# Optimization experiments

Measured on AMD Instinct MI355X. Metric: run time of the kernel, lower is better.

The kernel has to match this reference:

```python
import jax, jax.numpy as jnp
import numpy as np

B, H, L, V = 128, 1024, 60, 50257


def setup_inputs() -> dict:
    key = jax.random.key(0)
    ks = jax.random.split(key, 14)
    s = 0.02
    f32 = jnp.float32
    return {
        "input": jax.random.randint(ks[0], (B,), 0, V),
        "hidden": jax.random.normal(ks[1], (1, B, H), f32),
        "encoder_outputs": jax.random.normal(ks[2], (B, L, H), f32),
        # learned parameters
        "emb": (jax.random.normal(ks[3], (V, H), f32) * s),
        "attn_W": (jax.random.normal(ks[4], (L, 2 * H), f32) * s),
        "attn_b": jnp.zeros((L,), f32),
        "comb_W": (jax.random.normal(ks[5], (H, 2 * H), f32) * s),
        "comb_b": jnp.zeros((H,), f32),
        "W_ih": (jax.random.normal(ks[6], (3 * H, H), f32) * s),
        "W_hh": (jax.random.normal(ks[7], (3 * H, H), f32) * s),
        "b_ih": jnp.zeros((3 * H,), f32),
        "b_hh": jnp.zeros((3 * H,), f32),
        "out_W": (jax.random.normal(ks[8], (V, H), f32) * s),
        "out_b": jnp.zeros((V,), f32),
    }


def reference(input, hidden, encoder_outputs, emb, attn_W, attn_b,
              comb_W, comb_b, W_ih, W_hh, b_ih, b_hh, out_W, out_b):
    # embedding lookup (dropout is identity in eval mode)
    embedded = emb[input]                      # [B, H]
    h = hidden[0]                              # [B, H]

    # Bahdanau-style attention over fixed max_length positions
    attn_logits = jnp.concatenate([embedded, h], axis=1) @ attn_W.T + attn_b  # [B, L]
    attn_weights = jax.nn.softmax(attn_logits, axis=1)                        # [B, L]
    attn_applied = jnp.einsum('bl,blh->bh', attn_weights, encoder_outputs)    # [B, H]

    # combine + relu
    x = jnp.concatenate([embedded, attn_applied], axis=1) @ comb_W.T + comb_b  # [B, H]
    x = jax.nn.relu(x)

    # single GRU step (PyTorch gate order: r, z, n)
    gi = x @ W_ih.T + b_ih                     # [B, 3H]
    gh = h @ W_hh.T + b_hh                     # [B, 3H]
    i_r, i_z, i_n = jnp.split(gi, 3, axis=1)
    h_r, h_z, h_n = jnp.split(gh, 3, axis=1)
    r = jax.nn.sigmoid(i_r + h_r)
    z = jax.nn.sigmoid(i_z + h_z)
    n = jnp.tanh(i_n + r * h_n)
    h_new = (1.0 - z) * n + z * h              # [B, H]

    # output projection + log_softmax over vocab
    logp = jax.nn.log_softmax(h_new @ out_W.T + out_b, axis=1)  # [B, V]
    return logp, h_new[None], attn_weights
```

## Files before the change

kernel.cpp:

```cpp
#include <hip/hip_runtime.h>
#include <hip/hip_bf16.h>

#define B_ 128
#define H_ 1024
#define L_ 60
#define V_ 50257

typedef __attribute__((ext_vector_type(8))) short bf16x8;
typedef __attribute__((ext_vector_type(4))) float f32x4;

__device__ __forceinline__ unsigned short f2bf(float f) {
  union { __hip_bfloat16 h; unsigned short u; } v;
  v.h = __float2bfloat16(f);
  return v.u;
}

__device__ __forceinline__ bf16x8 cvt8(float4 a, float4 b) {
  union { bf16x8 v; __hip_bfloat16 h[8]; } u;
  u.h[0] = __float2bfloat16(a.x); u.h[1] = __float2bfloat16(a.y);
  u.h[2] = __float2bfloat16(a.z); u.h[3] = __float2bfloat16(a.w);
  u.h[4] = __float2bfloat16(b.x); u.h[5] = __float2bfloat16(b.y);
  u.h[6] = __float2bfloat16(b.z); u.h[7] = __float2bfloat16(b.w);
  return u.v;
}

#define SBAR()   __builtin_amdgcn_s_barrier()
#define SCHED0() __builtin_amdgcn_sched_barrier(0)
__device__ __forceinline__ void lwait0() { asm volatile("s_waitcnt lgkmcnt(0)" ::: "memory"); }

__device__ __forceinline__ size_t packIdx(int b, int k) {
  int s = k >> 5;
  int bm = b >> 4;
  int lane = (b & 15) | (((k >> 3) & 3) << 4);
  return ((size_t)((s * 8 + bm) * 64 + lane) << 3) | (size_t)(k & 7);
}

__global__ __launch_bounds__(256) void k_front(
    const int* __restrict__ input, const float* __restrict__ hidden,
    const float* __restrict__ emb, const float* __restrict__ attn_W,
    const float* __restrict__ attn_b, unsigned short* __restrict__ aXa,
    unsigned short* __restrict__ aH, float* __restrict__ lbuf)
{
  int bx = blockIdx.x;
  if (bx < 512) {
    int idx = bx * 256 + threadIdx.x;
    int b = idx >> 10, j = idx & (H_ - 1);
    float e = emb[(size_t)input[b] * H_ + j];
    float h = hidden[idx];
    size_t p = packIdx(b, j);
    aXa[p] = f2bf(e);
    aH[p]  = f2bf(h);
  } else {
    int t = threadIdx.x, wv = t >> 6, lane = t & 63;
    int task = (bx - 512) * 4 + wv;
    int b = task / L_, l = task - b * L_;
    const float* erow = emb + (size_t)input[b] * H_;
    const float* hrow = hidden + (size_t)b * H_;
    const float* wr = attn_W + (size_t)l * (2 * H_);
    float acc = 0.f;
    #pragma unroll 4
    for (int i = 0; i < 16; ++i) {
      int m = lane + i * 64;
      acc += erow[m] * wr[m] + hrow[m] * wr[H_ + m];
    }
    #pragma unroll
    for (int off = 32; off; off >>= 1) acc += __shfl_xor(acc, off);
    if (lane == 0) lbuf[b * 64 + l] = acc + attn_b[l];
  }
}

__global__ __launch_bounds__(256) void k_appsm(
    const float* __restrict__ enc, const float* __restrict__ lbuf,
    float* __restrict__ attnw, unsigned short* __restrict__ aXa)
{
  __shared__ float sWt[64];
  int b = blockIdx.x, q = blockIdx.y, t = threadIdx.x;
  if (t < 64) {
    float v = (t < L_) ? lbuf[b * 64 + t] : -1e30f;
    float m = v;
    #pragma unroll
    for (int off = 32; off; off >>= 1) m = fmaxf(m, __shfl_xor(m, off));
    float e = (t < L_) ? __expf(v - m) : 0.f;
    float s = e;
    #pragma unroll
    for (int off = 32; off; off >>= 1) s += __shfl_xor(s, off);
    float w = e / s;
    sWt[t] = w;
    if (q == 0 && t < L_) attnw[b * L_ + t] = w;
  }
  __syncthreads();
  int col = q * 256 + t;
  const float* eb = enc + (size_t)b * L_ * H_ + col;
  float acc = 0.f;
  #pragma unroll 4
  for (int l = 0; l < L_; ++l) acc += sWt[l] * eb[(size_t)l * H_];
  aXa[packIdx(b, H_ + col)] = f2bf(acc);
}

__global__ __launch_bounds__(256, 4) void k_gemm(
    const unsigned short* __restrict__ Apk, const unsigned short* __restrict__ Apk2,
    const float* __restrict__ Wt, const float* __restrict__ Wt2,
    const float* __restrict__ bias, float* __restrict__ Cdir,
    float* __restrict__ Cpart, float* __restrict__ Cpart2,
    float* __restrict__ pms, int K, int N, int nchunks, int halfY, int nblkx)
{
  __shared__ __align__(16) unsigned short bufW0[64 * 32];
  __shared__ __align__(16) unsigned short bufW1[64 * 32];
  int t = threadIdx.x, wv = t >> 6, lane = t & 63;
  int y = blockIdx.y;
  const unsigned short* A = Apk;
  const float* W = Wt;
  float* CP = Cpart;
  int sidx = y;
  if (halfY && y >= halfY) { A = Apk2; W = Wt2; CP = Cpart2; sidx = y - halfY; }
  int chunk0 = sidx * nchunks;
  int n0 = blockIdx.x * 64;
  int ch = wv & 1;
  int bm0 = (wv >> 1) * 4;
  int g = lane >> 4;

  int sr  = wv * 16 + (lane >> 2);
  int sj  = lane & 3;
  int ssl = sj ^ ((sr >> 1) & 3);
  int sgcol = n0 + sr; sgcol = (sgcol < N) ? sgcol : (N - 1);
  const float* wsrc = W + (size_t)sgcol * K + sj * 8;
  unsigned short* wdst0 = &bufW0[sr * 32 + ssl * 8];
  unsigned short* wdst1 = &bufW1[sr * 32 + ssl * 8];

  f32x4 acc[4][2];
  #pragma unroll
  for (int i = 0; i < 4; ++i)
    #pragma unroll
    for (int j = 0; j < 2; ++j) acc[i][j] = (f32x4){0.f, 0.f, 0.f, 0.f};

  auto GW = [&](int kc, float4& lo, float4& hi) {
    const float* p = wsrc + (size_t)kc * 32;
    lo = *(const float4*)p;
    hi = *(const float4*)(p + 4);
  };
  const bf16x8* apg = (const bf16x8*)A;
  auto LA = [&](int kc, bf16x8* x) {
    #pragma unroll
    for (int j = 0; j < 4; ++j)
      x[j] = apg[((size_t)kc * 8 + bm0 + j) * 64 + lane];
  };
  auto COMP = [&](const unsigned short* buf, const bf16x8* a) {
    #pragma unroll
    for (int nci = 0; nci < 2; ++nci) {
      int rr = (ch * 2 + nci) * 16 + (lane & 15);
      int s = g ^ ((rr >> 1) & 3);
      bf16x8 bfr = *(const bf16x8*)&buf[rr * 32 + s * 8];
      #pragma unroll
      for (int j = 0; j < 4; ++j)
        acc[j][nci] = __builtin_amdgcn_mfma_f32_16x16x32_bf16(a[j], bfr, acc[j][nci], 0, 0, 0);
    }
  };

  float4 lo0, hi0, lo1, hi1;
  bf16x8 aA[4], aB[4];
  GW(chunk0, lo0, hi0); LA(chunk0, aA);

  for (int kk = 0; kk < nchunks; kk += 2) {
    if (kk + 1 < nchunks) { GW(chunk0 + kk + 1, lo1, hi1); LA(chunk0 + kk + 1, aB); }
    *(bf16x8*)wdst0 = cvt8(lo0, hi0);
    lwait0(); SCHED0(); SBAR(); SCHED0();
    COMP(bufW0, aA);
    if (kk + 1 >= nchunks) break;
    if (kk + 2 < nchunks) { GW(chunk0 + kk + 2, lo0, hi0); LA(chunk0 + kk + 2, aA); }
    *(bf16x8*)wdst1 = cvt8(lo1, hi1);
    lwait0(); SCHED0(); SBAR(); SCHED0();
    COMP(bufW1, aB);
  }

  int cols[2]; float bv[2];
  #pragma unroll
  for (int nci = 0; nci < 2; ++nci) {
    int c = n0 + (ch * 2 + nci) * 16 + (lane & 15);
    cols[nci] = c;
    bv[nci] = (bias && c < N) ? bias[c] : 0.f;
  }
  int rb = (lane >> 4) * 4;
  if (CP) {
    float* dst = CP + (size_t)sidx * B_ * N;
    #pragma unroll
    for (int bm = 0; bm < 4; ++bm)
      #pragma unroll
      for (int r = 0; r < 4; ++r) {
        int row = (bm0 + bm) * 16 + rb + r;
        #pragma unroll
        for (int nci = 0; nci < 2; ++nci)
          if (cols[nci] < N) dst[(size_t)row * N + cols[nci]] = acc[bm][nci][r];
      }
  } else {
    #pragma unroll
    for (int bm = 0; bm < 4; ++bm)
      #pragma unroll
      for (int r = 0; r < 4; ++r) {
        int row = (bm0 + bm) * 16 + rb + r;
        #pragma unroll
        for (int nci = 0; nci < 2; ++nci)
          if (cols[nci] < N) Cdir[(size_t)row * N + cols[nci]] = acc[bm][nci][r] + bv[nci];
      }
    if (pms) {
      #pragma unroll
      for (int bm = 0; bm < 4; ++bm)
        #pragma unroll
        for (int r = 0; r < 4; ++r) {
          int row = (bm0 + bm) * 16 + rb + r;
          float m = -1e30f;
          #pragma unroll
          for (int nci = 0; nci < 2; ++nci)
            if (cols[nci] < N) m = fmaxf(m, acc[bm][nci][r] + bv[nci]);
          #pragma unroll
          for (int off = 8; off; off >>= 1) m = fmaxf(m, __shfl_xor(m, off));
          float e = 0.f;
          #pragma unroll
          for (int nci = 0; nci < 2; ++nci)
            if (cols[nci] < N) e += __expf(acc[bm][nci][r] + bv[nci] - m);
          #pragma unroll
          for (int off = 8; off; off >>= 1) e += __shfl_xor(e, off);
          if ((lane & 15) == 0) {
            size_t o = ((size_t)row * (2 * nblkx) + blockIdx.x * 2 + ch) * 2;
            pms[o] = m; pms[o + 1] = e;
          }
        }
    }
  }
}

__global__ __launch_bounds__(256) void k_reduce_comb(
    const float* __restrict__ parts, const float* __restrict__ bias,
    unsigned short* __restrict__ aX)
{
  int idx = blockIdx.x * 256 + threadIdx.x;
  int b = idx >> 10, j = idx & (H_ - 1);
  float s = bias[j];
  #pragma unroll
  for (int p = 0; p < 16; ++p) s += parts[(size_t)p * B_ * H_ + idx];
  s = fmaxf(s, 0.f);
  aX[packIdx(b, j)] = f2bf(s);
}

__global__ __launch_bounds__(256) void k_gate(
    const float* __restrict__ giP, const float* __restrict__ ghP,
    const float* __restrict__ b_ih, const float* __restrict__ b_hh,
    const float* __restrict__ hidden, float* __restrict__ hnew,
    unsigned short* __restrict__ aHn)
{
  int idx = blockIdx.x * 256 + threadIdx.x;
  int b = idx >> 10, j = idx & (H_ - 1);
  size_t base = (size_t)b * 3 * H_;
  float ir = b_ih[j], iz = b_ih[H_ + j], in_ = b_ih[2 * H_ + j];
  float hr = b_hh[j], hz = b_hh[H_ + j], hn = b_hh[2 * H_ + j];
  #pragma unroll
  for (int p = 0; p < 4; ++p) {
    const float* gi = giP + (size_t)p * B_ * 3 * H_ + base;
    const float* gh = ghP + (size_t)p * B_ * 3 * H_ + base;
    ir += gi[j]; iz += gi[H_ + j]; in_ += gi[2 * H_ + j];
    hr += gh[j]; hz += gh[H_ + j]; hn += gh[2 * H_ + j];
  }
  float r = 1.f / (1.f + __expf(-(ir + hr)));
  float z = 1.f / (1.f + __expf(-(iz + hz)));
  float n = tanhf(in_ + r * hn);
  float h = hidden[idx];
  float hv = (1.f - z) * n + z * h;
  hnew[idx] = hv;
  aHn[packIdx(b, j)] = f2bf(hv);
}

#define SL_ 6283
__global__ __launch_bounds__(256) void k_lsub(
    float* __restrict__ logits, const float* __restrict__ pms, int nblk2)
{
  __shared__ float sm[4], ss[4], sc;
  int b = blockIdx.x, sl = blockIdx.y, t = threadIdx.x;
  float M = -1e30f, S = 0.f;
  for (int i = t; i < nblk2; i += 256) {
    float m = pms[((size_t)b * nblk2 + i) * 2];
    float s = pms[((size_t)b * nblk2 + i) * 2 + 1];
    float nm = fmaxf(M, m);
    S = S * __expf(M - nm) + s * __expf(m - nm);
    M = nm;
  }
  #pragma unroll
  for (int off = 32; off; off >>= 1) {
    float m2 = __shfl_xor(M, off), s2 = __shfl_xor(S, off);
    float nm = fmaxf(M, m2);
    S = S * __expf(M - nm) + s2 * __expf(m2 - nm);
    M = nm;
  }
  if ((t & 63) == 0) { sm[t >> 6] = M; ss[t >> 6] = S; }
  __syncthreads();
  if (t == 0) {
    float Mf = sm[0], Sf = ss[0];
    #pragma unroll
    for (int i = 1; i < 4; ++i) {
      float nm = fmaxf(Mf, sm[i]);
      Sf = Sf * __expf(Mf - nm) + ss[i] * __expf(sm[i] - nm);
      Mf = nm;
    }
    sc = Mf + logf(Sf);
  }
  __syncthreads();
  float c = sc;
  int v0 = sl * SL_;
  int v1 = v0 + SL_; if (v1 > V_) v1 = V_;
  float* row = logits + (size_t)b * V_;
  for (int v = v0 + t; v < v1; v += 256) row[v] -= c;
}

extern "C" void kernel_launch(void* const* d_in, const int* in_sizes, int n_in,
                              void* d_out, int out_size, void* d_ws, size_t ws_size,
                              hipStream_t stream)
{
  const int*   input  = (const int*)d_in[0];
  const float* hidden = (const float*)d_in[1];
  const float* enc    = (const float*)d_in[2];
  const float* emb    = (const float*)d_in[3];
  const float* attn_W = (const float*)d_in[4];
  const float* attn_b = (const float*)d_in[5];
  const float* comb_W = (const float*)d_in[6];
  const float* comb_b = (const float*)d_in[7];
  const float* W_ih   = (const float*)d_in[8];
  const float* W_hh   = (const float*)d_in[9];
  const float* b_ih   = (const float*)d_in[10];
  const float* b_hh   = (const float*)d_in[11];
  const float* out_W  = (const float*)d_in[12];
  const float* out_b  = (const float*)d_in[13];

  float* out    = (float*)d_out;
  float* logits = out;
  float* hnew   = out + (size_t)B_ * V_;
  float* attnw  = hnew + (size_t)B_ * H_;

  const int NBLK = (V_ + 63) / 64;
  char* ws = (char*)d_ws;
  unsigned short* aXa = (unsigned short*)(ws);
  unsigned short* aH  = (unsigned short*)(ws + 524288);
  unsigned short* aX  = (unsigned short*)(ws + 786432);
  unsigned short* aHn = (unsigned short*)(ws + 1048576);
  float* lbuf  = (float*)(ws + 1310720);
  float* pms   = (float*)(ws + 1343488);
  float* combP = (float*)(ws + 4194304);
  float* giP   = (float*)(ws + 4194304);
  float* ghP   = (float*)(ws + 4194304 + 6291456);

  k_front<<<512 + (B_ * L_) / 4, 256, 0, stream>>>(input, hidden, emb, attn_W, attn_b,
                                                   aXa, aH, lbuf);
  k_appsm<<<dim3(B_, 4), 256, 0, stream>>>(enc, lbuf, attnw, aXa);
  k_gemm<<<dim3(16, 16), 256, 0, stream>>>(aXa, nullptr, comb_W, nullptr, nullptr,
                                           nullptr, combP, nullptr, nullptr,
                                           2 * H_, H_, 4, 0, 0);
  k_reduce_comb<<<(B_ * H_) / 256, 256, 0, stream>>>(combP, comb_b, aX);
  k_gemm<<<dim3(48, 8), 256, 0, stream>>>(aX, aH, W_ih, W_hh, nullptr,
                                          nullptr, giP, ghP, nullptr,
                                          H_, 3 * H_, 8, 4, 0);
  k_gate<<<(B_ * H_) / 256, 256, 0, stream>>>(giP, ghP, b_ih, b_hh, hidden, hnew, aHn);
  k_gemm<<<dim3(NBLK, 1), 256, 0, stream>>>(aHn, nullptr, out_W, nullptr, out_b,
                                            logits, nullptr, nullptr, pms,
                                            H_, V_, 32, 0, NBLK);
  k_lsub<<<dim3(B_, 8), 256, 0, stream>>>(logits, pms, 2 * NBLK);
}
```

Before: 131.9 us.

## Stage activations via global_load_lds and narrow GEMM tiles to 32 columns

The shared GEMM kernel now loads the packed bf16 activation tiles directly into LDS with global_load_lds instead of into registers. It runs a deeper 4-stage register prefetch of the fp32 weights, with vmcnt-based waits. The N tile shrinks from 64 to 32 columns, which doubles the block count for all three GEMMs, and launch bounds rise to 6 blocks per SM. The aim is better latency hiding and occupancy on the bandwidth-bound out_W projection, at the cost of more redundant activation traffic per block and more barriers. The pms buffer moves because it grows to hold twice as many partial entries.

```diff
diff --git a/kernel.cpp b/kernel.cpp
--- a/kernel.cpp
+++ b/kernel.cpp
@@ -7,6 +7,7 @@
 #define V_ 50257
 
 typedef __attribute__((ext_vector_type(8))) short bf16x8;
+typedef __attribute__((ext_vector_type(4))) short bf16x4;
 typedef __attribute__((ext_vector_type(4))) float f32x4;
 
 __device__ __forceinline__ unsigned short f2bf(float f) {
@@ -15,18 +16,17 @@
   return v.u;
 }
 
-__device__ __forceinline__ bf16x8 cvt8(float4 a, float4 b) {
-  union { bf16x8 v; __hip_bfloat16 h[8]; } u;
-  u.h[0] = __float2bfloat16(a.x); u.h[1] = __float2bfloat16(a.y);
-  u.h[2] = __float2bfloat16(a.z); u.h[3] = __float2bfloat16(a.w);
-  u.h[4] = __float2bfloat16(b.x); u.h[5] = __float2bfloat16(b.y);
-  u.h[6] = __float2bfloat16(b.z); u.h[7] = __float2bfloat16(b.w);
-  return u.v;
+__device__ __forceinline__ void gl_lds16(const void* g, void* l) {
+  __builtin_amdgcn_global_load_lds(
+      (const __attribute__((address_space(1))) unsigned int*)g,
+      (__attribute__((address_space(3))) unsigned int*)l, 16, 0, 0);
 }
 
 #define SBAR()   __builtin_amdgcn_s_barrier()
 #define SCHED0() __builtin_amdgcn_sched_barrier(0)
 __device__ __forceinline__ void lwait0() { asm volatile("s_waitcnt lgkmcnt(0)" ::: "memory"); }
+__device__ __forceinline__ void vwait4() { asm volatile("s_waitcnt vmcnt(4)" ::: "memory"); }
+__device__ __forceinline__ void vwait0() { asm volatile("s_waitcnt vmcnt(0)" ::: "memory"); }
 
 __device__ __forceinline__ size_t packIdx(int b, int k) {
   int s = k >> 5;
@@ -97,15 +97,15 @@
   aXa[packIdx(b, H_ + col)] = f2bf(acc);
 }
 
-__global__ __launch_bounds__(256, 4) void k_gemm(
+__global__ __launch_bounds__(256, 6) void k_gemm(
     const unsigned short* __restrict__ Apk, const unsigned short* __restrict__ Apk2,
     const float* __restrict__ Wt, const float* __restrict__ Wt2,
     const float* __restrict__ bias, float* __restrict__ Cdir,
     float* __restrict__ Cpart, float* __restrict__ Cpart2,
     float* __restrict__ pms, int K, int N, int nchunks, int halfY, int nblkx)
 {
-  __shared__ __align__(16) unsigned short bufW0[64 * 32];
-  __shared__ __align__(16) unsigned short bufW1[64 * 32];
+  __shared__ __align__(16) unsigned short bufW[2][32 * 32];
+  __shared__ __align__(16) unsigned short bufA[2][8 * 512];
   int t = threadIdx.x, wv = t >> 6, lane = t & 63;
   int y = blockIdx.y;
   const unsigned short* A = Apk;
@@ -114,71 +114,95 @@
   int sidx = y;
   if (halfY && y >= halfY) { A = Apk2; W = Wt2; CP = Cpart2; sidx = y - halfY; }
   int chunk0 = sidx * nchunks;
-  int n0 = blockIdx.x * 64;
+  int cend = chunk0 + nchunks;
+  int n0 = blockIdx.x * 32;
   int ch = wv & 1;
   int bm0 = (wv >> 1) * 4;
   int g = lane >> 4;
 
-  int sr  = wv * 16 + (lane >> 2);
-  int sj  = lane & 3;
-  int ssl = sj ^ ((sr >> 1) & 3);
-  int sgcol = n0 + sr; sgcol = (sgcol < N) ? sgcol : (N - 1);
-  const float* wsrc = W + (size_t)sgcol * K + sj * 8;
-  unsigned short* wdst0 = &bufW0[sr * 32 + ssl * 8];
-  unsigned short* wdst1 = &bufW1[sr * 32 + ssl * 8];
-
-  f32x4 acc[4][2];
+  int tr = t >> 3, tq = t & 7;
+  int wgcol = n0 + tr; if (wgcol >= N) wgcol = N - 1;
+  const float* wsrc = W + (size_t)wgcol * K + tq * 4;
+  int wsl = ((tq >> 1) ^ ((tr >> 1) & 3)) * 8 + (tq & 1) * 4;
+  unsigned short* wd0 = &bufW[0][tr * 32 + wsl];
+  unsigned short* wd1 = &bufW[1][tr * 32 + wsl];
+
+  f32x4 acc[4];
   #pragma unroll
-  for (int i = 0; i < 4; ++i)
-    #pragma unroll
-    for (int j = 0; j < 2; ++j) acc[i][j] = (f32x4){0.f, 0.f, 0.f, 0.f};
-
-  auto GW = [&](int kc, float4& lo, float4& hi) {
-    const float* p = wsrc + (size_t)kc * 32;
-    lo = *(const float4*)p;
-    hi = *(const float4*)(p + 4);
+  for (int i = 0; i < 4; ++i) acc[i] = (f32x4){0.f, 0.f, 0.f, 0.f};
+
+  auto GWl = [&](int kc) { return *(const float4*)(wsrc + (size_t)kc * 32); };
+  auto WST = [&](unsigned short* d, float4 w) {
+    bf16x4 v;
+    v[0] = (short)f2bf(w.x); v[1] = (short)f2bf(w.y);
+    v[2] = (short)f2bf(w.z); v[3] = (short)f2bf(w.w);
+    *(bf16x4*)d = v;
   };
-  const bf16x8* apg = (const bf16x8*)A;
-  auto LA = [&](int kc, bf16x8* x) {
-    #pragma unroll
-    for (int j = 0; j < 4; ++j)
-      x[j] = apg[((size_t)kc * 8 + bm0 + j) * 64 + lane];
+  auto GA = [&](int kc, unsigned short* bA) {
+    #pragma unroll
+    for (int f2 = 0; f2 < 2; ++f2) {
+      int f = wv * 2 + f2;
+      const unsigned short* src = A + ((size_t)kc * 8 + f) * 512 + lane * 8;
+      gl_lds16(src, bA + f * 512);
+    }
   };
-  auto COMP = [&](const unsigned short* buf, const bf16x8* a) {
-    #pragma unroll
-    for (int nci = 0; nci < 2; ++nci) {
-      int rr = (ch * 2 + nci) * 16 + (lane & 15);
-      int s = g ^ ((rr >> 1) & 3);
-      bf16x8 bfr = *(const bf16x8*)&buf[rr * 32 + s * 8];
-      #pragma unroll
-      for (int j = 0; j < 4; ++j)
-        acc[j][nci] = __builtin_amdgcn_mfma_f32_16x16x32_bf16(a[j], bfr, acc[j][nci], 0, 0, 0);
+  auto COMP = [&](const unsigned short* bW, const unsigned short* bA) {
+    int rr = ch * 16 + (lane & 15);
+    int sp = g ^ ((rr >> 1) & 3);
+    bf16x8 bfr = *(const bf16x8*)&bW[rr * 32 + sp * 8];
+    #pragma unroll
+    for (int bm = 0; bm < 4; ++bm) {
+      bf16x8 af = *(const bf16x8*)&bA[(bm0 + bm) * 512 + lane * 8];
+      acc[bm] = __builtin_amdgcn_mfma_f32_16x16x32_bf16(af, bfr, acc[bm], 0, 0, 0);
     }
   };
 
-  float4 lo0, hi0, lo1, hi1;
-  bf16x8 aA[4], aB[4];
-  GW(chunk0, lo0, hi0); LA(chunk0, aA);
-
-  for (int kk = 0; kk < nchunks; kk += 2) {
-    if (kk + 1 < nchunks) { GW(chunk0 + kk + 1, lo1, hi1); LA(chunk0 + kk + 1, aB); }
-    *(bf16x8*)wdst0 = cvt8(lo0, hi0);
-    lwait0(); SCHED0(); SBAR(); SCHED0();
-    COMP(bufW0, aA);
-    if (kk + 1 >= nchunks) break;
-    if (kk + 2 < nchunks) { GW(chunk0 + kk + 2, lo0, hi0); LA(chunk0 + kk + 2, aA); }
-    *(bf16x8*)wdst1 = cvt8(lo1, hi1);
-    lwait0(); SCHED0(); SBAR(); SCHED0();
-    COMP(bufW1, aB);
-  }
-
-  int cols[2]; float bv[2];
-  #pragma unroll
-  for (int nci = 0; nci < 2; ++nci) {
-    int c = n0 + (ch * 2 + nci) * 16 + (lane & 15);
-    cols[nci] = c;
-    bv[nci] = (bias && c < N) ? bias[c] : 0.f;
-  }
+  float4 wreg[4];
+  wreg[0] = GWl(chunk0);
+  wreg[1] = GWl(chunk0 + 1);
+  SCHED0();
+  GA(chunk0, bufA[0]);
+  GA(chunk0 + 1, bufA[1]);
+  SCHED0();
+  wreg[2] = GWl(chunk0 + 2);
+  wreg[3] = GWl(chunk0 + 3);
+  SCHED0();
+  WST(wd0, wreg[0]);
+  WST(wd1, wreg[1]);
+  lwait0(); vwait4(); SCHED0(); SBAR();
+
+  int c = chunk0;
+  for (; c + 8 <= cend; c += 4) {
+    #pragma unroll
+    for (int hh = 0; hh < 4; ++hh) {
+      COMP(bufW[hh & 1], bufA[hh & 1]);
+      SCHED0(); SBAR(); SCHED0();
+      GA(c + hh + 2, bufA[hh & 1]);
+      SCHED0();
+      wreg[hh] = GWl(c + hh + 4);
+      SCHED0();
+      WST((hh & 1) ? wd1 : wd0, wreg[(hh + 2) & 3]);
+      lwait0(); vwait4(); SCHED0(); SBAR();
+    }
+  }
+
+  {
+    COMP(bufW[0], bufA[0]);
+    SCHED0(); SBAR(); SCHED0();
+    GA(c + 2, bufA[0]);
+    WST(wd0, wreg[2]);
+    lwait0(); vwait0(); SCHED0(); SBAR();
+    COMP(bufW[1], bufA[1]);
+    SCHED0(); SBAR(); SCHED0();
+    GA(c + 3, bufA[1]);
+    WST(wd1, wreg[3]);
+    lwait0(); vwait0(); SCHED0(); SBAR();
+    COMP(bufW[0], bufA[0]);
+    COMP(bufW[1], bufA[1]);
+  }
+
+  int col = n0 + ch * 16 + (lane & 15);
+  float bv = (bias && col < N) ? bias[col] : 0.f;
   int rb = (lane >> 4) * 4;
   if (CP) {
     float* dst = CP + (size_t)sidx * B_ * N;
@@ -187,9 +211,7 @@
       #pragma unroll
       for (int r = 0; r < 4; ++r) {
         int row = (bm0 + bm) * 16 + rb + r;
-        #pragma unroll
-        for (int nci = 0; nci < 2; ++nci)
-          if (cols[nci] < N) dst[(size_t)row * N + cols[nci]] = acc[bm][nci][r];
+        if (col < N) dst[(size_t)row * N + col] = acc[bm][r];
       }
   } else {
     #pragma unroll
@@ -197,9 +219,7 @@
       #pragma unroll
       for (int r = 0; r < 4; ++r) {
         int row = (bm0 + bm) * 16 + rb + r;
-        #pragma unroll
-        for (int nci = 0; nci < 2; ++nci)
-          if (cols[nci] < N) Cdir[(size_t)row * N + cols[nci]] = acc[bm][nci][r] + bv[nci];
+        if (col < N) Cdir[(size_t)row * N + col] = acc[bm][r] + bv;
       }
     if (pms) {
       #pragma unroll
@@ -207,16 +227,10 @@
         #pragma unroll
         for (int r = 0; r < 4; ++r) {
           int row = (bm0 + bm) * 16 + rb + r;
-          float m = -1e30f;
-          #pragma unroll
-          for (int nci = 0; nci < 2; ++nci)
-            if (cols[nci] < N) m = fmaxf(m, acc[bm][nci][r] + bv[nci]);
+          float m = (col < N) ? (acc[bm][r] + bv) : -1e30f;
           #pragma unroll
           for (int off = 8; off; off >>= 1) m = fmaxf(m, __shfl_xor(m, off));
-          float e = 0.f;
-          #pragma unroll
-          for (int nci = 0; nci < 2; ++nci)
-            if (cols[nci] < N) e += __expf(acc[bm][nci][r] + bv[nci] - m);
+          float e = (col < N) ? __expf(acc[bm][r] + bv - m) : 0.f;
           #pragma unroll
           for (int off = 8; off; off >>= 1) e += __shfl_xor(e, off);
           if ((lane & 15) == 0) {
@@ -333,26 +347,26 @@
   float* hnew   = out + (size_t)B_ * V_;
   float* attnw  = hnew + (size_t)B_ * H_;
 
-  const int NBLK = (V_ + 63) / 64;
+  const int NBLK = (V_ + 31) / 32;
   char* ws = (char*)d_ws;
   unsigned short* aXa = (unsigned short*)(ws);
   unsigned short* aH  = (unsigned short*)(ws + 524288);
   unsigned short* aX  = (unsigned short*)(ws + 786432);
   unsigned short* aHn = (unsigned short*)(ws + 1048576);
   float* lbuf  = (float*)(ws + 1310720);
-  float* pms   = (float*)(ws + 1343488);
   float* combP = (float*)(ws + 4194304);
   float* giP   = (float*)(ws + 4194304);
   float* ghP   = (float*)(ws + 4194304 + 6291456);
+  float* pms   = (float*)(ws + 20971520);
 
   k_front<<<512 + (B_ * L_) / 4, 256, 0, stream>>>(input, hidden, emb, attn_W, attn_b,
                                                    aXa, aH, lbuf);
   k_appsm<<<dim3(B_, 4), 256, 0, stream>>>(enc, lbuf, attnw, aXa);
-  k_gemm<<<dim3(16, 16), 256, 0, stream>>>(aXa, nullptr, comb_W, nullptr, nullptr,
+  k_gemm<<<dim3(32, 16), 256, 0, stream>>>(aXa, nullptr, comb_W, nullptr, nullptr,
                                            nullptr, combP, nullptr, nullptr,
                                            2 * H_, H_, 4, 0, 0);
   k_reduce_comb<<<(B_ * H_) / 256, 256, 0, stream>>>(combP, comb_b, aX);
-  k_gemm<<<dim3(48, 8), 256, 0, stream>>>(aX, aH, W_ih, W_hh, nullptr,
+  k_gemm<<<dim3(96, 8), 256, 0, stream>>>(aX, aH, W_ih, W_hh, nullptr,
                                           nullptr, giP, ghP, nullptr,
                                           H_, 3 * H_, 8, 4, 0);
   k_gate<<<(B_ * H_) / 256, 256, 0, stream>>>(giP, ghP, b_ih, b_hh, hidden, hnew, aHn);
```

Result: slower. 146.0 us (+10.7%).

## Prepack output weights into MFMA fragment layout in chunks before vocab GEMM

Applied to the files above, without the earlier changes.

Replaces the generic vocab-projection GEMM with a two-stage scheme. A pack kernel converts out_W to bf16 in an MFMA-fragment-ordered layout, and a specialized GEMM streams those fragments with a software-pipelined load/compute loop. The work is done in four vocab chunks so the packed buffer fits in workspace and stays cache-resident between pack and consume. It adds extra kernel launches and a full fp32 read plus bf16 write and read of the weights, in exchange for simpler, coalesced operand loads in the GEMM.

```diff
diff --git a/kernel.cpp b/kernel.cpp
--- a/kernel.cpp
+++ b/kernel.cpp
@@ -5,6 +5,7 @@
 #define H_ 1024
 #define L_ 60
 #define V_ 50257
+#define NM_ 3142
 
 typedef __attribute__((ext_vector_type(8))) short bf16x8;
 typedef __attribute__((ext_vector_type(4))) float f32x4;
@@ -201,31 +202,99 @@
         for (int nci = 0; nci < 2; ++nci)
           if (cols[nci] < N) Cdir[(size_t)row * N + cols[nci]] = acc[bm][nci][r] + bv[nci];
       }
-    if (pms) {
+  }
+}
+
+__global__ __launch_bounds__(256) void k_wpack(
+    const float* __restrict__ W, unsigned short* __restrict__ Bq,
+    int nm0, int Krow)
+{
+  __shared__ float sW[16][132];
+  int t = threadIdx.x;
+  int nml = blockIdx.x, sg = blockIdx.y;
+  int nmg = nm0 + nml;
+  int r = t >> 4, seg = t & 15;
+  int row = nmg * 16 + r;
+  int k0 = sg * 128 + seg * 8;
+  float4 lo = {0.f,0.f,0.f,0.f}, hi = lo;
+  if (row < V_) {
+    const float* p = W + (size_t)row * Krow + k0;
+    lo = *(const float4*)p;
+    hi = *(const float4*)(p + 4);
+  }
+  *(float4*)&sW[r][seg * 8]     = lo;
+  *(float4*)&sW[r][seg * 8 + 4] = hi;
+  __syncthreads();
+  int wv = t >> 6, lane = t & 63;
+  int g = lane >> 4;
+  float4 a = *(const float4*)&sW[lane & 15][wv * 32 + g * 8];
+  float4 b = *(const float4*)&sW[lane & 15][wv * 32 + g * 8 + 4];
+  size_t fi = ((size_t)nml * 32 + sg * 4 + wv) * 512 + (size_t)lane * 8;
+  *(bf16x8*)&Bq[fi] = cvt8(a, b);
+}
+
+__global__ __launch_bounds__(256, 4) void k_pgemm(
+    const unsigned short* __restrict__ Apk, const unsigned short* __restrict__ Bq,
+    const float* __restrict__ bias, float* __restrict__ logits,
+    float* __restrict__ pms, int nm0)
+{
+  int t = threadIdx.x, wv = t >> 6, lane = t & 63;
+  int nml2 = blockIdx.x * 2;
+  int ch = wv & 1;
+  int bm0 = (wv >> 1) * 4;
+  int nmg = nm0 + nml2 + ch;
+  const bf16x8* bp  = (const bf16x8*)Bq + ((size_t)(nml2 + ch) * 32) * 64 + lane;
+  const bf16x8* apg = (const bf16x8*)Apk + lane;
+
+  f32x4 acc[4];
+  #pragma unroll
+  for (int i = 0; i < 4; ++i) acc[i] = (f32x4){0.f, 0.f, 0.f, 0.f};
+
+#define PLOAD(c, bw, a) {                                   \
+    bw = bp[(c) * 64];                                      \
+    _Pragma("unroll")                                       \
+    for (int j_ = 0; j_ < 4; ++j_)                          \
+      a[j_] = apg[(((c) * 8) + bm0 + j_) * 64]; }
+#define PCOMP(bw, a) {                                      \
+    _Pragma("unroll")                                       \
+    for (int j_ = 0; j_ < 4; ++j_)                          \
+      acc[j_] = __builtin_amdgcn_mfma_f32_16x16x32_bf16(a[j_], bw, acc[j_], 0, 0, 0); }
+
+  bf16x8 bA, bB, bC, bD;
+  bf16x8 aA[4], aB[4], aC[4], aD[4];
+  PLOAD(0, bA, aA); PLOAD(1, bB, aB); PLOAD(2, bC, aC); PLOAD(3, bD, aD);
+  SCHED0();
+  for (int c = 0; c + 8 <= 32; c += 4) {
+    PCOMP(bA, aA); PLOAD(c + 4, bA, aA); SCHED0();
+    PCOMP(bB, aB); PLOAD(c + 5, bB, aB); SCHED0();
+    PCOMP(bC, aC); PLOAD(c + 6, bC, aC); SCHED0();
+    PCOMP(bD, aD); PLOAD(c + 7, bD, aD); SCHED0();
+  }
+  PCOMP(bA, aA); PCOMP(bB, aB); PCOMP(bC, aC); PCOMP(bD, aD);
+#undef PLOAD
+#undef PCOMP
+
+  int col = nmg * 16 + (lane & 15);
+  float bv = (col < V_) ? bias[col] : 0.f;
+  int rb = (lane >> 4) * 4;
+  #pragma unroll
+  for (int bm = 0; bm < 4; ++bm)
+    #pragma unroll
+    for (int r = 0; r < 4; ++r) {
+      int row = (bm0 + bm) * 16 + rb + r;
+      float v = acc[bm][r] + bv;
+      if (col < V_) logits[(size_t)row * V_ + col] = v;
+      float m = (col < V_) ? v : -1e30f;
       #pragma unroll
-      for (int bm = 0; bm < 4; ++bm)
-        #pragma unroll
-        for (int r = 0; r < 4; ++r) {
-          int row = (bm0 + bm) * 16 + rb + r;
-          float m = -1e30f;
-          #pragma unroll
-          for (int nci = 0; nci < 2; ++nci)
-            if (cols[nci] < N) m = fmaxf(m, acc[bm][nci][r] + bv[nci]);
-          #pragma unroll
-          for (int off = 8; off; off >>= 1) m = fmaxf(m, __shfl_xor(m, off));
-          float e = 0.f;
-          #pragma unroll
-          for (int nci = 0; nci < 2; ++nci)
-            if (cols[nci] < N) e += __expf(acc[bm][nci][r] + bv[nci] - m);
-          #pragma unroll
-          for (int off = 8; off; off >>= 1) e += __shfl_xor(e, off);
-          if ((lane & 15) == 0) {
-            size_t o = ((size_t)row * (2 * nblkx) + blockIdx.x * 2 + ch) * 2;
-            pms[o] = m; pms[o + 1] = e;
-          }
-        }
+      for (int off = 8; off; off >>= 1) m = fmaxf(m, __shfl_xor(m, off));
+      float e = (col < V_) ? __expf(v - m) : 0.f;
+      #pragma unroll
+      for (int off = 8; off; off >>= 1) e += __shfl_xor(e, off);
+      if ((lane & 15) == 0) {
+        size_t o = ((size_t)row * NM_ + nmg) * 2;
+        pms[o] = m; pms[o + 1] = e;
+      }
     }
-  }
 }
 
 __global__ __launch_bounds__(256) void k_reduce_comb(
@@ -333,7 +402,6 @@
   float* hnew   = out + (size_t)B_ * V_;
   float* attnw  = hnew + (size_t)B_ * H_;
 
-  const int NBLK = (V_ + 63) / 64;
   char* ws = (char*)d_ws;
   unsigned short* aXa = (unsigned short*)(ws);
   unsigned short* aH  = (unsigned short*)(ws + 524288);
@@ -341,9 +409,10 @@
   unsigned short* aHn = (unsigned short*)(ws + 1048576);
   float* lbuf  = (float*)(ws + 1310720);
   float* pms   = (float*)(ws + 1343488);
-  float* combP = (float*)(ws + 4194304);
-  float* giP   = (float*)(ws + 4194304);
-  float* ghP   = (float*)(ws + 4194304 + 6291456);
+  float* combP = (float*)(ws + 4587520);
+  float* giP   = (float*)(ws + 4587520);
+  float* ghP   = (float*)(ws + 4587520 + 6291456);
+  unsigned short* Bq = (unsigned short*)(ws + 4587520);
 
   k_front<<<512 + (B_ * L_) / 4, 256, 0, stream>>>(input, hidden, emb, attn_W, attn_b,
                                                    aXa, aH, lbuf);
@@ -356,8 +425,11 @@
                                           nullptr, giP, ghP, nullptr,
                                           H_, 3 * H_, 8, 4, 0);
   k_gate<<<(B_ * H_) / 256, 256, 0, stream>>>(giP, ghP, b_ih, b_hh, hidden, hnew, aHn);
-  k_gemm<<<dim3(NBLK, 1), 256, 0, stream>>>(aHn, nullptr, out_W, nullptr, out_b,
-                                            logits, nullptr, nullptr, pms,
-                                            H_, V_, 32, 0, NBLK);
-  k_lsub<<<dim3(B_, 8), 256, 0, stream>>>(logits, pms, 2 * NBLK);
-}
+  for (int q = 0; q < 4; ++q) {
+    int nm0 = q * 786;
+    int nmq = (q == 3) ? (NM_ - 3 * 786) : 786;
+    k_wpack<<<dim3(nmq, 8), 256, 0, stream>>>(out_W, Bq, nm0, H_);
+    k_pgemm<<<nmq / 2, 256, 0, stream>>>(aHn, Bq, out_b, logits, pms, nm0);
+  }
+  k_lsub<<<dim3(B_, 8), 256, 0, stream>>>(logits, pms, NM_);
+}
```

New measurement: 209.4 us. 1.59x slower.

## Add dedicated vocab projection kernel with larger K tiles and swizzled LDS

Applied to the files above, without the earlier changes.

Replaces the generic GEMM path for the vocabulary output projection with a new k_proj kernel. It uses 512 threads, stages 256-wide K chunks of out_W in double-buffered, XOR-swizzled LDS, and has each wave compute a 16-column by 64-row tile. Partial max/sum-exp statistics are emitted per 16-column group, so the log-softmax reducer now reads NPB_*4 partials. The aim is fewer barriers and better latency hiding on the dominant weight-streaming GEMM. In exchange it uses much more LDS per block (64 KB), which may limit occupancy, and it reads the A fragments directly from global memory inside the MFMA loop.

```diff
diff --git a/kernel.cpp b/kernel.cpp
--- a/kernel.cpp
+++ b/kernel.cpp
@@ -5,8 +5,11 @@
 #define H_ 1024
 #define L_ 60
 #define V_ 50257
+#define NPB_ 786
+#define NMP_ (NPB_ * 4)
 
 typedef __attribute__((ext_vector_type(8))) short bf16x8;
+typedef __attribute__((ext_vector_type(4))) short bf16x4;
 typedef __attribute__((ext_vector_type(4))) float f32x4;
 
 __device__ __forceinline__ unsigned short f2bf(float f) {
@@ -22,6 +25,13 @@
   u.h[4] = __float2bfloat16(b.x); u.h[5] = __float2bfloat16(b.y);
   u.h[6] = __float2bfloat16(b.z); u.h[7] = __float2bfloat16(b.w);
   return u.v;
+}
+
+__device__ __forceinline__ bf16x4 cvt4(float4 a) {
+  bf16x4 v;
+  v[0] = (short)f2bf(a.x); v[1] = (short)f2bf(a.y);
+  v[2] = (short)f2bf(a.z); v[3] = (short)f2bf(a.w);
+  return v;
 }
 
 #define SBAR()   __builtin_amdgcn_s_barrier()
@@ -100,9 +110,8 @@
 __global__ __launch_bounds__(256, 4) void k_gemm(
     const unsigned short* __restrict__ Apk, const unsigned short* __restrict__ Apk2,
     const float* __restrict__ Wt, const float* __restrict__ Wt2,
-    const float* __restrict__ bias, float* __restrict__ Cdir,
     float* __restrict__ Cpart, float* __restrict__ Cpart2,
-    float* __restrict__ pms, int K, int N, int nchunks, int halfY, int nblkx)
+    int K, int N, int nchunks, int halfY)
 {
   __shared__ __align__(16) unsigned short bufW0[64 * 32];
   __shared__ __align__(16) unsigned short bufW1[64 * 32];
@@ -172,60 +181,109 @@
     COMP(bufW1, aB);
   }
 
-  int cols[2]; float bv[2];
-  #pragma unroll
-  for (int nci = 0; nci < 2; ++nci) {
-    int c = n0 + (ch * 2 + nci) * 16 + (lane & 15);
-    cols[nci] = c;
-    bv[nci] = (bias && c < N) ? bias[c] : 0.f;
-  }
+  float* dst = CP + (size_t)sidx * B_ * N;
   int rb = (lane >> 4) * 4;
-  if (CP) {
-    float* dst = CP + (size_t)sidx * B_ * N;
-    #pragma unroll
-    for (int bm = 0; bm < 4; ++bm)
+  #pragma unroll
+  for (int bm = 0; bm < 4; ++bm)
+    #pragma unroll
+    for (int r = 0; r < 4; ++r) {
+      int row = (bm0 + bm) * 16 + rb + r;
       #pragma unroll
-      for (int r = 0; r < 4; ++r) {
-        int row = (bm0 + bm) * 16 + rb + r;
-        #pragma unroll
-        for (int nci = 0; nci < 2; ++nci)
-          if (cols[nci] < N) dst[(size_t)row * N + cols[nci]] = acc[bm][nci][r];
+      for (int nci = 0; nci < 2; ++nci) {
+        int c = n0 + (ch * 2 + nci) * 16 + (lane & 15);
+        if (c < N) dst[(size_t)row * N + c] = acc[bm][nci][r];
       }
-  } else {
-    #pragma unroll
-    for (int bm = 0; bm < 4; ++bm)
+    }
+}
+
+__global__ __launch_bounds__(512, 4) void k_proj(
+    const unsigned short* __restrict__ Apk, const float* __restrict__ W,
+    const float* __restrict__ bias, float* __restrict__ logits,
+    float* __restrict__ pms)
+{
+  __shared__ __align__(16) unsigned short bufW[2][64 * 256];
+  int t = threadIdx.x, w = t >> 6, lane = t & 63;
+  int n0 = blockIdx.x * 64;
+  int mh = w >> 2, cg = w & 3;
+  int bm0 = mh * 4;
+
+  int srow0 = w * 8;
+  const bf16x8* apg = (const bf16x8*)Apk;
+
+  f32x4 acc[4];
+  #pragma unroll
+  for (int i = 0; i < 4; ++i) acc[i] = (f32x4){0.f, 0.f, 0.f, 0.f};
+
+  auto LD = [&](int c, float4* rg) {
+    #pragma unroll
+    for (int i = 0; i < 8; ++i) {
+      int rr = srow0 + i;
+      int gr = n0 + rr; gr = (gr < V_) ? gr : (V_ - 1);
+      rg[i] = *(const float4*)(W + (size_t)gr * H_ + c * 256 + lane * 4);
+    }
+  };
+  auto WR = [&](int bi, const float4* rg) {
+    #pragma unroll
+    for (int i = 0; i < 8; ++i) {
+      int rr = srow0 + i;
+      int off = rr * 256 + (((lane >> 1) ^ (rr & 7)) << 3) + ((lane & 1) << 2);
+      *(bf16x4*)&bufW[bi][off] = cvt4(rg[i]);
+    }
+  };
+  auto COMP = [&](int bi, int c) {
+    int rr = cg * 16 + (lane & 15);
+    #pragma unroll
+    for (int ks = 0; ks < 8; ++ks) {
+      int phys = ((ks << 2) + (lane >> 4)) ^ (lane & 7);
+      bf16x8 bw = *(const bf16x8*)&bufW[bi][rr * 256 + (phys << 3)];
+      int s = c * 8 + ks;
       #pragma unroll
-      for (int r = 0; r < 4; ++r) {
-        int row = (bm0 + bm) * 16 + rb + r;
-        #pragma unroll
-        for (int nci = 0; nci < 2; ++nci)
-          if (cols[nci] < N) Cdir[(size_t)row * N + cols[nci]] = acc[bm][nci][r] + bv[nci];
+      for (int bm = 0; bm < 4; ++bm) {
+        bf16x8 af = apg[((size_t)s * 8 + bm0 + bm) * 64 + lane];
+        acc[bm] = __builtin_amdgcn_mfma_f32_16x16x32_bf16(af, bw, acc[bm], 0, 0, 0);
       }
-    if (pms) {
+    }
+  };
+
+  float4 rA[8], rB[8];
+  LD(0, rA);
+  LD(1, rB);
+  WR(0, rA);
+  lwait0(); SCHED0(); SBAR(); SCHED0();
+  LD(2, rA);
+  COMP(0, 0);
+  WR(1, rB);
+  lwait0(); SCHED0(); SBAR(); SCHED0();
+  LD(3, rB);
+  COMP(1, 1);
+  WR(0, rA);
+  lwait0(); SCHED0(); SBAR(); SCHED0();
+  COMP(0, 2);
+  WR(1, rB);
+  lwait0(); SCHED0(); SBAR(); SCHED0();
+  COMP(1, 3);
+
+  int col = n0 + cg * 16 + (lane & 15);
+  float bv = (col < V_) ? bias[col] : 0.f;
+  int rb = (lane >> 4) * 4;
+  #pragma unroll
+  for (int bm = 0; bm < 4; ++bm)
+    #pragma unroll
+    for (int r = 0; r < 4; ++r) {
+      int row = mh * 64 + bm * 16 + rb + r;
+      float v = acc[bm][r] + bv;
+      if (col < V_) logits[(size_t)row * V_ + col] = v;
+      float m = (col < V_) ? v : -1e30f;
       #pragma unroll
-      for (int bm = 0; bm < 4; ++bm)
-        #pragma unroll
-        for (int r = 0; r < 4; ++r) {
-          int row = (bm0 + bm) * 16 + rb + r;
-          float m = -1e30f;
-          #pragma unroll
-          for (int nci = 0; nci < 2; ++nci)
-            if (cols[nci] < N) m = fmaxf(m, acc[bm][nci][r] + bv[nci]);
-          #pragma unroll
-          for (int off = 8; off; off >>= 1) m = fmaxf(m, __shfl_xor(m, off));
-          float e = 0.f;
-          #pragma unroll
-          for (int nci = 0; nci < 2; ++nci)
-            if (cols[nci] < N) e += __expf(acc[bm][nci][r] + bv[nci] - m);
-          #pragma unroll
-          for (int off = 8; off; off >>= 1) e += __shfl_xor(e, off);
-          if ((lane & 15) == 0) {
-            size_t o = ((size_t)row * (2 * nblkx) + blockIdx.x * 2 + ch) * 2;
-            pms[o] = m; pms[o + 1] = e;
-          }
-        }
-    }
-  }
+      for (int off = 8; off; off >>= 1) m = fmaxf(m, __shfl_xor(m, off));
+      float e = (col < V_) ? __expf(v - m) : 0.f;
+      #pragma unroll
+      for (int off = 8; off; off >>= 1) e += __shfl_xor(e, off);
+      if ((lane & 15) == 0) {
+        size_t o = ((size_t)row * NMP_ + blockIdx.x * 4 + cg) * 2;
+        pms[o] = m; pms[o + 1] = e;
+      }
+    }
 }
 
 __global__ __launch_bounds__(256) void k_reduce_comb(
@@ -333,7 +391,6 @@
   float* hnew   = out + (size_t)B_ * V_;
   float* attnw  = hnew + (size_t)B_ * H_;
 
-  const int NBLK = (V_ + 63) / 64;
   char* ws = (char*)d_ws;
   unsigned short* aXa = (unsigned short*)(ws);
   unsigned short* aH  = (unsigned short*)(ws + 524288);
@@ -341,23 +398,19 @@
   unsigned short* aHn = (unsigned short*)(ws + 1048576);
   float* lbuf  = (float*)(ws + 1310720);
   float* pms   = (float*)(ws + 1343488);
-  float* combP = (float*)(ws + 4194304);
-  float* giP   = (float*)(ws + 4194304);
-  float* ghP   = (float*)(ws + 4194304 + 6291456);
+  float* combP = (float*)(ws + 4587520);
+  float* giP   = (float*)(ws + 4587520);
+  float* ghP   = (float*)(ws + 4587520 + 6291456);
 
   k_front<<<512 + (B_ * L_) / 4, 256, 0, stream>>>(input, hidden, emb, attn_W, attn_b,
                                                    aXa, aH, lbuf);
   k_appsm<<<dim3(B_, 4), 256, 0, stream>>>(enc, lbuf, attnw, aXa);
-  k_gemm<<<dim3(16, 16), 256, 0, stream>>>(aXa, nullptr, comb_W, nullptr, nullptr,
-                                           nullptr, combP, nullptr, nullptr,
-                                           2 * H_, H_, 4, 0, 0);
+  k_gemm<<<dim3(16, 16), 256, 0, stream>>>(aXa, nullptr, comb_W, nullptr,
+                                           combP, nullptr, 2 * H_, H_, 4, 0);
   k_reduce_comb<<<(B_ * H_) / 256, 256, 0, stream>>>(combP, comb_b, aX);
-  k_gemm<<<dim3(48, 8), 256, 0, stream>>>(aX, aH, W_ih, W_hh, nullptr,
-                                          nullptr, giP, ghP, nullptr,
-                                          H_, 3 * H_, 8, 4, 0);
+  k_gemm<<<dim3(48, 8), 256, 0, stream>>>(aX, aH, W_ih, W_hh,
+                                          giP, ghP, H_, 3 * H_, 8, 4);
   k_gate<<<(B_ * H_) / 256, 256, 0, stream>>>(giP, ghP, b_ih, b_hh, hidden, hnew, aHn);
-  k_gemm<<<dim3(NBLK, 1), 256, 0, stream>>>(aHn, nullptr, out_W, nullptr, out_b,
-                                            logits, nullptr, nullptr, pms,
-                                            H_, V_, 32, 0, NBLK);
-  k_lsub<<<dim3(B_, 8), 256, 0, stream>>>(logits, pms, 2 * NBLK);
-}
+  k_proj<<<NPB_, 512, 0, stream>>>(aHn, out_W, out_b, logits, pms);
+  k_lsub<<<dim3(B_, 8), 256, 0, stream>>>(logits, pms, NMP_);
+}
```

After: 157.2 us. 1.19x slower.
